# Optimization experiments

Measured on AMD Instinct MI355X. Metric: run time of the kernel, lower is better.

Reference implementation:

```python
import jax, jax.numpy as jnp
import numpy as np

K = 20000   # know_num
I = 50000   # item_num
D = 128     # emb_dim
N = K + I   # nodes in exer+know graphs (exercises first)
E1 = 320000 # edges in directed knowledge graph
E2 = 640000 # edges in each exer<->know graph


def setup_inputs() -> dict:
    key = jax.random.key(0)
    ks = jax.random.split(key, 20)
    s = 1.0 / np.sqrt(D)
    s2 = 1.0 / np.sqrt(2 * D)
    return {
        'kn_emb': jax.random.normal(ks[0], (K, D), jnp.float32),
        'exer_emb': jax.random.normal(ks[1], (I, D), jnp.float32),
        # GAT params: W is fc.weight.T ([in,out]); a is attn_fc.weight flattened ([2D])
        'W_dir': jax.random.normal(ks[2], (D, D), jnp.float32) * s,
        'a_dir': jax.random.normal(ks[3], (2 * D,), jnp.float32) * s2,
        'W_ke': jax.random.normal(ks[4], (D, D), jnp.float32) * s,
        'a_ke': jax.random.normal(ks[5], (2 * D,), jnp.float32) * s2,
        'W_ek': jax.random.normal(ks[6], (D, D), jnp.float32) * s,
        'a_ek': jax.random.normal(ks[7], (2 * D,), jnp.float32) * s2,
        # relation attention MLP: Linear(D,D)+bias, Tanh, Linear(D,1,no bias)
        'rel_W1': jax.random.normal(ks[8], (D, D), jnp.float32) * s,
        'rel_b1': jax.random.normal(ks[9], (D,), jnp.float32) * s,
        'rel_w2': jax.random.normal(ks[10], (D,), jnp.float32) * s,
        # edge lists (src, dst)
        'directed_src': jax.random.randint(ks[11], (E1,), 0, K),
        'directed_dst': jax.random.randint(ks[12], (E1,), 0, K),
        'ke_src': jax.random.randint(ks[13], (E2,), 0, N),
        'ke_dst': jax.random.randint(ks[14], (E2,), 0, N),
        'ek_src': jax.random.randint(ks[15], (E2,), 0, N),
        'ek_dst': jax.random.randint(ks[16], (E2,), 0, N),
    }


def _gat(h, W, a, src, dst, n):
    # GraphLayer: z = fc(h); e = leaky_relu(attn_fc([z_src; z_dst]));
    # alpha = softmax_e over dst; h_out = sum alpha * z_src
    z = h @ W                                   # [n_in, D]
    # split attn vector: cat([z_src,z_dst]) @ a == z_src@a[:D] + z_dst@a[D:]
    s_src = z @ a[:D]                           # [n_in]
    s_dst = z @ a[D:]                           # [n_in]
    e = jax.nn.leaky_relu(s_src[src] + s_dst[dst], 0.01)  # [E]
    m = jax.ops.segment_max(e, dst, num_segments=n)
    ex = jnp.exp(e - m[dst])
    den = jax.ops.segment_sum(ex, dst, num_segments=n)
    alpha = ex / den[dst]                       # segment softmax over in-edges
    return jax.ops.segment_sum(alpha[:, None] * z[src], dst, num_segments=n)


def reference(kn_emb, exer_emb, W_dir, a_dir, W_ke, a_ke, W_ek, a_ek,
              rel_W1, rel_b1, rel_w2,
              directed_src, directed_dst, ke_src, ke_dst, ek_src, ek_dst):
    A = _gat(kn_emb, W_dir, a_dir, directed_src, directed_dst, K)      # [K,D]
    ek = jnp.concatenate([exer_emb, kn_emb], axis=0)                   # [N,D]
    B = _gat(ek, W_ke, a_ke, ke_src, ke_dst, N)[I:]                    # [K,D]
    Cfull = _gat(ek, W_ek, a_ek, ek_src, ek_dst, N)                    # [N,D]
    s1 = jnp.tanh(A @ rel_W1 + rel_b1) @ rel_w2                        # [K]
    s2 = jnp.tanh(B @ rel_W1 + rel_b1) @ rel_w2                        # [K]
    score = jax.nn.softmax(jnp.stack([s1, s2], axis=1), axis=1)        # [K,2]
    kn_out = score[:, 0:1] * A + score[:, 1:2] * B                     # [K,D]
    exer_out = Cfull[:I]                                               # [I,D]
    return (kn_out, exer_out)
```

## Files before the change

kernel.cpp:

```cpp
#include <hip/hip_runtime.h>
#include <math.h>

#define KN   20000
#define IN_  50000
#define DD   128
#define NN   70000
#define E1N  320000
#define E2N  640000

#define GB0  313
#define GB1  1094
#define GB2  1094

typedef _Float16 f16x8 __attribute__((ext_vector_type(8)));
typedef float floatx4 __attribute__((ext_vector_type(4)));

__device__ __forceinline__ unsigned f2bf(float x) {
  unsigned u = __float_as_uint(x);
  return (u + 0x7FFFu + ((u >> 16) & 1u)) >> 16;
}
__device__ __forceinline__ unsigned packbf(float a, float b) {
  return f2bf(a) | (f2bf(b) << 16);
}
__device__ __forceinline__ float bf_lo(unsigned u) { return __uint_as_float(u << 16); }
__device__ __forceinline__ float bf_hi(unsigned u) { return __uint_as_float(u & 0xFFFF0000u); }

__global__ __launch_bounds__(256) void prep(
    const float* __restrict__ W0, const float* __restrict__ W1,
    const float* __restrict__ W2, const float* __restrict__ W3,
    short* __restrict__ wfr,
    const int* __restrict__ ddst, const int* __restrict__ kedst, const int* __restrict__ ekdst,
    int* __restrict__ cnt_dir, int* __restrict__ cnt_ke, int* __restrict__ cnt_ek,
    unsigned short* __restrict__ rank_dir, unsigned short* __restrict__ rank_ke,
    unsigned short* __restrict__ rank_ek)
{
  int b = blockIdx.x;
  if (b < 32) {
    int wsel = b >> 3;
    const float* W = (wsel == 0) ? W0 : (wsel == 1) ? W1 : (wsel == 2) ? W2 : W3;
    int fi = (b & 7) * 256 + threadIdx.x;
    int l = fi & 63, chunk = (fi >> 6) & 3, t = fi >> 8;
    int col = t * 16 + (l & 15);
    int kbase = chunk * 32 + (l >> 4) * 8;
    f16x8 hv;
#pragma unroll
    for (int j = 0; j < 8; ++j) hv[j] = (_Float16)W[(kbase + j) * 128 + col];
    ((f16x8*)(wfr + wsel * 16384))[fi] = hv;
    return;
  }
  int i = (b - 32) * 256 + threadIdx.x;
  if (i < E1N) {
    rank_dir[i] = (unsigned short)atomicAdd(&cnt_dir[ddst[i]], 1);
  } else if (i < E1N + E2N) {
    int e = i - E1N;
    int d = kedst[e];
    if (d >= IN_) rank_ke[e] = (unsigned short)atomicAdd(&cnt_ke[d - IN_], 1);
  } else {
    int e = i - E1N - E2N;
    int d = ekdst[e];
    if (d < IN_) rank_ek[e] = (unsigned short)atomicAdd(&cnt_ek[d], 1);
  }
}

__global__ __launch_bounds__(256, 4) void gemm3(
    const float* __restrict__ kn, const float* __restrict__ ex,
    const short* __restrict__ wfr,
    const float* __restrict__ a_dir, const float* __restrict__ a_ke, const float* __restrict__ a_ek,
    unsigned* __restrict__ zb_dir, unsigned* __restrict__ zb_ke, unsigned* __restrict__ zb_ek,
    float* __restrict__ sds, float* __restrict__ sdd,
    float* __restrict__ sks, float* __restrict__ skd,
    float* __restrict__ ses, float* __restrict__ sed)
{
  __shared__ short sW[16384];
  const int bid = blockIdx.x;
  const int tid = threadIdx.x;

  const float *h1, *h2, *avec;
  unsigned* zb;
  float *ssrc, *sdst;
  const short* wf;
  int split, rows, tile;
  if (bid < GB0) {
    tile = bid; rows = KN; split = KN; h1 = kn; h2 = kn;
    wf = wfr; avec = a_dir; zb = zb_dir; ssrc = sds; sdst = sdd;
  } else if (bid < GB0 + GB1) {
    tile = bid - GB0; rows = NN; split = IN_; h1 = ex; h2 = kn;
    wf = wfr + 16384; avec = a_ke; zb = zb_ke; ssrc = sks; sdst = skd;
  } else {
    tile = bid - GB0 - GB1; rows = NN; split = IN_; h1 = ex; h2 = kn;
    wf = wfr + 32768; avec = a_ek; zb = zb_ek; ssrc = ses; sdst = sed;
  }

  {
    const int4* gs = (const int4*)wf;
    int4* ls = (int4*)sW;
#pragma unroll
    for (int it = 0; it < 8; ++it) ls[it * 256 + tid] = gs[it * 256 + tid];
  }
  __syncthreads();

  const int lane = tid & 63;
  const int wv = tid >> 6;
  const int q = lane >> 4;
  const int m = lane & 15;
  const int r = tile * 64 + wv * 16 + m;
  const int rc = (r < rows) ? r : (rows - 1);
  const float* hp = (rc < split) ? (h1 + (size_t)rc * 128)
                                 : (h2 + (size_t)(rc - split) * 128);

  floatx4 acc[8];
#pragma unroll
  for (int t = 0; t < 8; ++t) { acc[t][0]=0.f; acc[t][1]=0.f; acc[t][2]=0.f; acc[t][3]=0.f; }

#pragma unroll
  for (int chunk = 0; chunk < 4; ++chunk) {
    float4 v0 = *(const float4*)(hp + chunk * 32 + q * 8);
    float4 v1 = *(const float4*)(hp + chunk * 32 + q * 8 + 4);
    float vs[8] = {v0.x, v0.y, v0.z, v0.w, v1.x, v1.y, v1.z, v1.w};
    f16x8 ahi, alo;
#pragma unroll
    for (int j = 0; j < 8; ++j) {
      _Float16 h = (_Float16)vs[j];
      ahi[j] = h;
      alo[j] = (_Float16)(vs[j] - (float)h);
    }
#pragma unroll
    for (int t = 0; t < 8; ++t) {
      f16x8 bh = ((const f16x8*)sW)[(t * 4 + chunk) * 64 + lane];
      acc[t] = __builtin_amdgcn_mfma_f32_16x16x32_f16(bh, ahi, acc[t], 0, 0, 0);
      acc[t] = __builtin_amdgcn_mfma_f32_16x16x32_f16(bh, alo, acc[t], 0, 0, 0);
    }
  }

  if (r < rows) {
    unsigned* zrow = zb + (size_t)r * 64;
#pragma unroll
    for (int t = 0; t < 8; ++t) {
      uint2 pk;
      pk.x = packbf(acc[t][0], acc[t][1]);
      pk.y = packbf(acc[t][2], acc[t][3]);
      *(uint2*)(zrow + t * 8 + q * 2) = pk;
    }
  }
  float d1 = 0.f, d2 = 0.f;
#pragma unroll
  for (int t = 0; t < 8; ++t) {
    float4 wa = *(const float4*)(avec + t * 16 + q * 4);
    float4 wb = *(const float4*)(avec + 128 + t * 16 + q * 4);
    d1 += acc[t][0] * wa.x + acc[t][1] * wa.y + acc[t][2] * wa.z + acc[t][3] * wa.w;
    d2 += acc[t][0] * wb.x + acc[t][1] * wb.y + acc[t][2] * wb.z + acc[t][3] * wb.w;
  }
  d1 += __shfl_xor(d1, 16, 64); d1 += __shfl_xor(d1, 32, 64);
  d2 += __shfl_xor(d2, 16, 64); d2 += __shfl_xor(d2, 32, 64);
  if (q == 0 && r < rows) { ssrc[r] = d1; sdst[r] = d2; }
}

__global__ __launch_bounds__(256) void alloc_off(
    const int* __restrict__ cnt_dir, int* __restrict__ st_dir,
    const int* __restrict__ cnt_ke,  int* __restrict__ st_ke,
    const int* __restrict__ cnt_ek,  int* __restrict__ st_ek,
    int* __restrict__ totals)
{
  int b = blockIdx.x;
  const int* cnt; int* st; int* tot; int n, i0;
  if (b < 79)       { cnt = cnt_dir; st = st_dir; tot = totals + 0; n = KN;  i0 = b * 256; }
  else if (b < 158) { cnt = cnt_ke;  st = st_ke;  tot = totals + 1; n = KN;  i0 = (b - 79) * 256; }
  else              { cnt = cnt_ek;  st = st_ek;  tot = totals + 2; n = IN_; i0 = (b - 158) * 256; }
  int i = i0 + threadIdx.x;
  int lane = threadIdx.x & 63;
  int v = (i < n) ? cnt[i] : 0;
  int x = v;
#pragma unroll
  for (int o = 1; o < 64; o <<= 1) {
    int t = __shfl_up(x, o, 64);
    if (lane >= o) x += t;
  }
  int base = 0;
  if (lane == 63) base = atomicAdd(tot, x);
  base = __shfl(base, 63, 64);
  if (i < n) st[i] = base + x - v;
}

__global__ __launch_bounds__(256) void fill_edges(
    const int* __restrict__ dsrc, const int* __restrict__ ddst,
    const int* __restrict__ kesrc, const int* __restrict__ kedst,
    const int* __restrict__ eksrc, const int* __restrict__ ekdst,
    const unsigned short* __restrict__ rank_dir, const unsigned short* __restrict__ rank_ke,
    const unsigned short* __restrict__ rank_ek,
    const float* __restrict__ sds, const float* __restrict__ sks, const float* __restrict__ ses,
    const int* __restrict__ st_dir, int2* __restrict__ ep_dir,
    const int* __restrict__ st_ke,  int2* __restrict__ ep_ke,
    const int* __restrict__ st_ek,  int2* __restrict__ ep_ek)
{
  int i = blockIdx.x * 256 + threadIdx.x;
  if (i < E1N) {
    int d = ddst[i];
    int s = dsrc[i];
    ep_dir[st_dir[d] + rank_dir[i]] = make_int2(s, __float_as_int(sds[s]));
  } else if (i < E1N + E2N) {
    int e = i - E1N;
    int d = kedst[e];
    if (d >= IN_) {
      int s = kesrc[e];
      ep_ke[st_ke[d - IN_] + rank_ke[e]] = make_int2(s, __float_as_int(sks[s]));
    }
  } else {
    int e = i - E1N - E2N;
    int d = ekdst[e];
    if (d < IN_) {
      int s = eksrc[e];
      ep_ek[st_ek[d] + rank_ek[e]] = make_int2(s, __float_as_int(ses[s]));
    }
  }
}

__global__ __launch_bounds__(256) void gat_gather(
    const int* __restrict__ st_dir, const int* __restrict__ cnt_dir, const int2* __restrict__ ep_dir,
    const float* __restrict__ sdd, const unsigned* __restrict__ zb_dir, float* __restrict__ A,
    const int* __restrict__ st_ke, const int* __restrict__ cnt_ke, const int2* __restrict__ ep_ke,
    const float* __restrict__ skd, const unsigned* __restrict__ zb_ke, float* __restrict__ Bm,
    const int* __restrict__ st_ek, const int* __restrict__ cnt_ek, const int2* __restrict__ ep_ek,
    const float* __restrict__ sed, const unsigned* __restrict__ zb_ek, float* __restrict__ Cout)
{
  int w = (blockIdx.x * 256 + threadIdx.x) >> 6;
  int lane = threadIdx.x & 63;
  int gid = lane >> 4, gl = lane & 15;
  const int *st, *cn; const int2* ep;
  const float* sD;
  const unsigned* zb;
  float* out;
  int seg, node;
  if (w < KN)                { seg = w;          node = seg;       st = st_dir; cn = cnt_dir; ep = ep_dir; sD = sdd; zb = zb_dir; out = A; }
  else if (w < 2 * KN)       { seg = w - KN;     node = seg + IN_; st = st_ke;  cn = cnt_ke;  ep = ep_ke;  sD = skd; zb = zb_ke;  out = Bm; }
  else if (w < 2 * KN + IN_) { seg = w - 2 * KN; node = seg;       st = st_ek;  cn = cnt_ek;  ep = ep_ek;  sD = sed; zb = zb_ek;  out = Cout; }
  else return;

  int b = st[seg], e = b + cn[seg];
  float av[8];
#pragma unroll
  for (int k = 0; k < 8; ++k) av[k] = 0.f;
  float den = 0.f;

  if (e > b) {
    float sd = sD[node];
    int i = b + gid;
    for (; i + 4 < e; i += 8) {
      int2 p1 = ep[i], p2 = ep[i + 4];
      float x1 = __int_as_float(p1.y) + sd; x1 = (x1 > 0.f) ? x1 : 0.01f * x1;
      float x2 = __int_as_float(p2.y) + sd; x2 = (x2 > 0.f) ? x2 : 0.01f * x2;
      float w1 = __expf(x1), w2 = __expf(x2);
      uint4 za = *(const uint4*)(zb + (size_t)p1.x * 64 + gl * 4);
      uint4 zc = *(const uint4*)(zb + (size_t)p2.x * 64 + gl * 4);
      den += w1 + w2;
      av[0] += w1 * bf_lo(za.x); av[1] += w1 * bf_hi(za.x);
      av[2] += w1 * bf_lo(za.y); av[3] += w1 * bf_hi(za.y);
      av[4] += w1 * bf_lo(za.z); av[5] += w1 * bf_hi(za.z);
      av[6] += w1 * bf_lo(za.w); av[7] += w1 * bf_hi(za.w);
      av[0] += w2 * bf_lo(zc.x); av[1] += w2 * bf_hi(zc.x);
      av[2] += w2 * bf_lo(zc.y); av[3] += w2 * bf_hi(zc.y);
      av[4] += w2 * bf_lo(zc.z); av[5] += w2 * bf_hi(zc.z);
      av[6] += w2 * bf_lo(zc.w); av[7] += w2 * bf_hi(zc.w);
    }
    if (i < e) {
      int2 p1 = ep[i];
      float x1 = __int_as_float(p1.y) + sd; x1 = (x1 > 0.f) ? x1 : 0.01f * x1;
      float w1 = __expf(x1);
      uint4 za = *(const uint4*)(zb + (size_t)p1.x * 64 + gl * 4);
      den += w1;
      av[0] += w1 * bf_lo(za.x); av[1] += w1 * bf_hi(za.x);
      av[2] += w1 * bf_lo(za.y); av[3] += w1 * bf_hi(za.y);
      av[4] += w1 * bf_lo(za.z); av[5] += w1 * bf_hi(za.z);
      av[6] += w1 * bf_lo(za.w); av[7] += w1 * bf_hi(za.w);
    }
    den += __shfl_xor(den, 16, 64);
    den += __shfl_xor(den, 32, 64);
#pragma unroll
    for (int k = 0; k < 8; ++k) {
      av[k] += __shfl_xor(av[k], 16, 64);
      av[k] += __shfl_xor(av[k], 32, 64);
    }
    float inv = 1.f / den;
#pragma unroll
    for (int k = 0; k < 8; ++k) av[k] *= inv;
  }

  if (gid == 0) {
    float* op = out + (size_t)seg * 128 + gl * 8;
    *(float4*)op       = make_float4(av[0], av[1], av[2], av[3]);
    *(float4*)(op + 4) = make_float4(av[4], av[5], av[6], av[7]);
  }
}

__global__ __launch_bounds__(256, 2) void relgemm_combine(
    const float* __restrict__ Am, const float* __restrict__ Bm,
    const short* __restrict__ wfr_rel,
    const float* __restrict__ rb1, const float* __restrict__ rw2,
    float* __restrict__ out)
{
  __shared__ short sW[16384];
  const int tid = threadIdx.x;
  {
    const int4* gs = (const int4*)wfr_rel;
    int4* ls = (int4*)sW;
#pragma unroll
    for (int it = 0; it < 8; ++it) ls[it * 256 + tid] = gs[it * 256 + tid];
  }
  __syncthreads();

  const int lane = tid & 63;
  const int wv = tid >> 6;
  const int q = lane >> 4;
  const int m = lane & 15;
  const int r = blockIdx.x * 64 + wv * 16 + m;
  const int rc = (r < KN) ? r : (KN - 1);
  const float* hA = Am + (size_t)rc * 128;
  const float* hB = Bm + (size_t)rc * 128;

  floatx4 accA[8], accB[8];
#pragma unroll
  for (int t = 0; t < 8; ++t) {
    accA[t][0]=0.f; accA[t][1]=0.f; accA[t][2]=0.f; accA[t][3]=0.f;
    accB[t][0]=0.f; accB[t][1]=0.f; accB[t][2]=0.f; accB[t][3]=0.f;
  }

#pragma unroll
  for (int chunk = 0; chunk < 4; ++chunk) {
    float4 a0 = *(const float4*)(hA + chunk * 32 + q * 8);
    float4 a1 = *(const float4*)(hA + chunk * 32 + q * 8 + 4);
    float4 b0 = *(const float4*)(hB + chunk * 32 + q * 8);
    float4 b1 = *(const float4*)(hB + chunk * 32 + q * 8 + 4);
    float as[8] = {a0.x, a0.y, a0.z, a0.w, a1.x, a1.y, a1.z, a1.w};
    float bs[8] = {b0.x, b0.y, b0.z, b0.w, b1.x, b1.y, b1.z, b1.w};
    f16x8 ahiA, aloA, ahiB, aloB;
#pragma unroll
    for (int j = 0; j < 8; ++j) {
      _Float16 ha = (_Float16)as[j];
      ahiA[j] = ha; aloA[j] = (_Float16)(as[j] - (float)ha);
      _Float16 hb = (_Float16)bs[j];
      ahiB[j] = hb; aloB[j] = (_Float16)(bs[j] - (float)hb);
    }
#pragma unroll
    for (int t = 0; t < 8; ++t) {
      f16x8 bh = ((const f16x8*)sW)[(t * 4 + chunk) * 64 + lane];
      accA[t] = __builtin_amdgcn_mfma_f32_16x16x32_f16(bh, ahiA, accA[t], 0, 0, 0);
      accA[t] = __builtin_amdgcn_mfma_f32_16x16x32_f16(bh, aloA, accA[t], 0, 0, 0);
      accB[t] = __builtin_amdgcn_mfma_f32_16x16x32_f16(bh, ahiB, accB[t], 0, 0, 0);
      accB[t] = __builtin_amdgcn_mfma_f32_16x16x32_f16(bh, aloB, accB[t], 0, 0, 0);
    }
  }

  float p1 = 0.f, p2 = 0.f;
#pragma unroll
  for (int t = 0; t < 8; ++t) {
    float4 bb = *(const float4*)(rb1 + t * 16 + q * 4);
    float4 ww = *(const float4*)(rw2 + t * 16 + q * 4);
    p1 += tanhf(accA[t][0] + bb.x) * ww.x + tanhf(accA[t][1] + bb.y) * ww.y +
          tanhf(accA[t][2] + bb.z) * ww.z + tanhf(accA[t][3] + bb.w) * ww.w;
    p2 += tanhf(accB[t][0] + bb.x) * ww.x + tanhf(accB[t][1] + bb.y) * ww.y +
          tanhf(accB[t][2] + bb.z) * ww.z + tanhf(accB[t][3] + bb.w) * ww.w;
  }
  p1 += __shfl_xor(p1, 16, 64); p1 += __shfl_xor(p1, 32, 64);
  p2 += __shfl_xor(p2, 16, 64); p2 += __shfl_xor(p2, 32, 64);

  float mx = fmaxf(p1, p2);
  float e1 = __expf(p1 - mx), e2 = __expf(p2 - mx);
  float al = e1 / (e1 + e2), be = e2 / (e1 + e2);

  if (r < KN) {
#pragma unroll
    for (int t = 0; t < 8; ++t) {
      int col = t * 16 + q * 4;
      float4 avv = *(const float4*)(Am + (size_t)r * 128 + col);
      float4 bvv = *(const float4*)(Bm + (size_t)r * 128 + col);
      *(float4*)(out + (size_t)r * 128 + col) =
          make_float4(al * avv.x + be * bvv.x, al * avv.y + be * bvv.y,
                      al * avv.z + be * bvv.z, al * avv.w + be * bvv.w);
    }
  }
}

extern "C" void kernel_launch(void* const* d_in, const int* in_sizes, int n_in,
                              void* d_out, int out_size, void* d_ws, size_t ws_size,
                              hipStream_t stream) {
  const float* kn    = (const float*)d_in[0];
  const float* ex    = (const float*)d_in[1];
  const float* W_dir = (const float*)d_in[2];
  const float* a_dir = (const float*)d_in[3];
  const float* W_ke  = (const float*)d_in[4];
  const float* a_ke  = (const float*)d_in[5];
  const float* W_ek  = (const float*)d_in[6];
  const float* a_ek  = (const float*)d_in[7];
  const float* rW1   = (const float*)d_in[8];
  const float* rb1   = (const float*)d_in[9];
  const float* rw2   = (const float*)d_in[10];
  const int* dsrc    = (const int*)d_in[11];
  const int* ddst    = (const int*)d_in[12];
  const int* kesrc   = (const int*)d_in[13];
  const int* kedst   = (const int*)d_in[14];
  const int* eksrc   = (const int*)d_in[15];
  const int* ekdst   = (const int*)d_in[16];
  float* out = (float*)d_out;

  char* p = (char*)d_ws;
  auto alloc = [&](size_t bytes) {
    char* r = p;
    p += (bytes + 255) & ~(size_t)255;
    return r;
  };
  unsigned* zb_dir = (unsigned*)alloc((size_t)KN * 64 * 4);
  unsigned* zb_ke  = (unsigned*)alloc((size_t)NN * 64 * 4);
  unsigned* zb_ek  = (unsigned*)alloc((size_t)NN * 64 * 4);
  float* Am    = (float*)alloc((size_t)KN * 128 * 4);
  float* Bmat  = (float*)alloc((size_t)KN * 128 * 4);
  short* wfr   = (short*)alloc((size_t)4 * 16384 * 2);
  float* sds = (float*)alloc(KN * 4);
  float* sdd = (float*)alloc(KN * 4);
  float* sks = (float*)alloc(NN * 4);
  float* skd = (float*)alloc(NN * 4);
  float* ses = (float*)alloc(NN * 4);
  float* sed = (float*)alloc(NN * 4);
  int* cntblk  = (int*)alloc((size_t)(2 * KN + IN_ + 64) * 4);
  int* cnt_dir = cntblk;
  int* cnt_ke  = cntblk + KN;
  int* cnt_ek  = cntblk + 2 * KN;
  int* totals  = cntblk + 2 * KN + IN_;
  int* st_dir = (int*)alloc(KN * 4);
  int* st_ke  = (int*)alloc(KN * 4);
  int* st_ek  = (int*)alloc(IN_ * 4);
  unsigned short* rank_dir = (unsigned short*)alloc((size_t)E1N * 2);
  unsigned short* rank_ke  = (unsigned short*)alloc((size_t)E2N * 2);
  unsigned short* rank_ek  = (unsigned short*)alloc((size_t)E2N * 2);
  int2* ep_dir = (int2*)alloc((size_t)E1N * 8);
  int2* ep_ke  = (int2*)alloc((size_t)E2N * 8);
  int2* ep_ek  = (int2*)alloc((size_t)E2N * 8);

  hipMemsetAsync(cntblk, 0, (size_t)(2 * KN + IN_ + 64) * 4, stream);

  prep<<<32 + (E1N + 2 * E2N) / 256, 256, 0, stream>>>(
      W_dir, W_ke, W_ek, rW1, wfr,
      ddst, kedst, ekdst, cnt_dir, cnt_ke, cnt_ek,
      rank_dir, rank_ke, rank_ek);

  gemm3<<<GB0 + GB1 + GB2, 256, 0, stream>>>(
      kn, ex, wfr, a_dir, a_ke, a_ek,
      zb_dir, zb_ke, zb_ek,
      sds, sdd, sks, skd, ses, sed);

  alloc_off<<<354, 256, 0, stream>>>(cnt_dir, st_dir, cnt_ke, st_ke, cnt_ek, st_ek, totals);

  fill_edges<<<(E1N + 2 * E2N) / 256, 256, 0, stream>>>(
      dsrc, ddst, kesrc, kedst, eksrc, ekdst,
      rank_dir, rank_ke, rank_ek,
      sds, sks, ses,
      st_dir, ep_dir, st_ke, ep_ke, st_ek, ep_ek);

  gat_gather<<<(2 * KN + IN_) / 4, 256, 0, stream>>>(
      st_dir, cnt_dir, ep_dir, sdd, zb_dir, Am,
      st_ke,  cnt_ke,  ep_ke,  skd, zb_ke,  Bmat,
      st_ek,  cnt_ek,  ep_ek,  sed, zb_ek,  out + (size_t)KN * 128);

  relgemm_combine<<<313, 256, 0, stream>>>(Am, Bmat, wfr + 3 * 16384, rb1, rw2, out);
}
```

Measured before the change: 283.6 us.

## Precompute edge softmax weights in fill and gather with 16-lane groups per segment

fill_edges now evaluates leaky_relu and exp per edge using both source and destination scores, and stores the final weight in the edge record. This removes the destination-score lookup and exp from the gather. gat_gather switches from one wavefront per destination segment (four interleaved edge streams plus shuffle reductions) to one 16-lane group per segment. Each group walks its edges serially with 16-byte paired edge loads, packed float2 accumulation and no cross-lane reduction. relgemm_combine keeps the A/B row values it already loaded in registers for the final blend instead of reloading them, at the cost of more register pressure.

```diff
diff --git a/kernel.cpp b/kernel.cpp
--- a/kernel.cpp
+++ b/kernel.cpp
@@ -14,6 +14,7 @@
 
 typedef _Float16 f16x8 __attribute__((ext_vector_type(8)));
 typedef float floatx4 __attribute__((ext_vector_type(4)));
+typedef float floatx2 __attribute__((ext_vector_type(2)));
 
 __device__ __forceinline__ unsigned f2bf(float x) {
   unsigned u = __float_as_uint(x);
@@ -24,6 +25,9 @@
 }
 __device__ __forceinline__ float bf_lo(unsigned u) { return __uint_as_float(u << 16); }
 __device__ __forceinline__ float bf_hi(unsigned u) { return __uint_as_float(u & 0xFFFF0000u); }
+__device__ __forceinline__ floatx2 bfp(unsigned u) {
+  floatx2 r; r.x = bf_lo(u); r.y = bf_hi(u); return r;
+}
 
 __global__ __launch_bounds__(256) void prep(
     const float* __restrict__ W0, const float* __restrict__ W1,
@@ -187,7 +191,9 @@
     const int* __restrict__ eksrc, const int* __restrict__ ekdst,
     const unsigned short* __restrict__ rank_dir, const unsigned short* __restrict__ rank_ke,
     const unsigned short* __restrict__ rank_ek,
-    const float* __restrict__ sds, const float* __restrict__ sks, const float* __restrict__ ses,
+    const float* __restrict__ sds, const float* __restrict__ sdd,
+    const float* __restrict__ sks, const float* __restrict__ skd,
+    const float* __restrict__ ses, const float* __restrict__ sed,
     const int* __restrict__ st_dir, int2* __restrict__ ep_dir,
     const int* __restrict__ st_ke,  int2* __restrict__ ep_ke,
     const int* __restrict__ st_ek,  int2* __restrict__ ep_ek)
@@ -196,99 +202,84 @@
   if (i < E1N) {
     int d = ddst[i];
     int s = dsrc[i];
-    ep_dir[st_dir[d] + rank_dir[i]] = make_int2(s, __float_as_int(sds[s]));
+    float x = sds[s] + sdd[d];
+    x = (x > 0.f) ? x : 0.01f * x;
+    ep_dir[st_dir[d] + rank_dir[i]] = make_int2(s, __float_as_int(__expf(x)));
   } else if (i < E1N + E2N) {
     int e = i - E1N;
     int d = kedst[e];
     if (d >= IN_) {
       int s = kesrc[e];
-      ep_ke[st_ke[d - IN_] + rank_ke[e]] = make_int2(s, __float_as_int(sks[s]));
+      float x = sks[s] + skd[d];
+      x = (x > 0.f) ? x : 0.01f * x;
+      ep_ke[st_ke[d - IN_] + rank_ke[e]] = make_int2(s, __float_as_int(__expf(x)));
     }
   } else {
     int e = i - E1N - E2N;
     int d = ekdst[e];
     if (d < IN_) {
       int s = eksrc[e];
-      ep_ek[st_ek[d] + rank_ek[e]] = make_int2(s, __float_as_int(ses[s]));
+      float x = ses[s] + sed[d];
+      x = (x > 0.f) ? x : 0.01f * x;
+      ep_ek[st_ek[d] + rank_ek[e]] = make_int2(s, __float_as_int(__expf(x)));
     }
   }
 }
 
 __global__ __launch_bounds__(256) void gat_gather(
     const int* __restrict__ st_dir, const int* __restrict__ cnt_dir, const int2* __restrict__ ep_dir,
-    const float* __restrict__ sdd, const unsigned* __restrict__ zb_dir, float* __restrict__ A,
+    const unsigned* __restrict__ zb_dir, float* __restrict__ A,
     const int* __restrict__ st_ke, const int* __restrict__ cnt_ke, const int2* __restrict__ ep_ke,
-    const float* __restrict__ skd, const unsigned* __restrict__ zb_ke, float* __restrict__ Bm,
+    const unsigned* __restrict__ zb_ke, float* __restrict__ Bm,
     const int* __restrict__ st_ek, const int* __restrict__ cnt_ek, const int2* __restrict__ ep_ek,
-    const float* __restrict__ sed, const unsigned* __restrict__ zb_ek, float* __restrict__ Cout)
-{
-  int w = (blockIdx.x * 256 + threadIdx.x) >> 6;
-  int lane = threadIdx.x & 63;
-  int gid = lane >> 4, gl = lane & 15;
+    const unsigned* __restrict__ zb_ek, float* __restrict__ Cout)
+{
+  int g = (blockIdx.x * 256 + threadIdx.x) >> 4;
+  int gl = threadIdx.x & 15;
   const int *st, *cn; const int2* ep;
-  const float* sD;
   const unsigned* zb;
   float* out;
-  int seg, node;
-  if (w < KN)                { seg = w;          node = seg;       st = st_dir; cn = cnt_dir; ep = ep_dir; sD = sdd; zb = zb_dir; out = A; }
-  else if (w < 2 * KN)       { seg = w - KN;     node = seg + IN_; st = st_ke;  cn = cnt_ke;  ep = ep_ke;  sD = skd; zb = zb_ke;  out = Bm; }
-  else if (w < 2 * KN + IN_) { seg = w - 2 * KN; node = seg;       st = st_ek;  cn = cnt_ek;  ep = ep_ek;  sD = sed; zb = zb_ek;  out = Cout; }
+  int seg;
+  if (g < KN)                { seg = g;          st = st_dir; cn = cnt_dir; ep = ep_dir; zb = zb_dir; out = A; }
+  else if (g < 2 * KN)       { seg = g - KN;     st = st_ke;  cn = cnt_ke;  ep = ep_ke;  zb = zb_ke;  out = Bm; }
+  else if (g < 2 * KN + IN_) { seg = g - 2 * KN; st = st_ek;  cn = cnt_ek;  ep = ep_ek;  zb = zb_ek;  out = Cout; }
   else return;
 
-  int b = st[seg], e = b + cn[seg];
-  float av[8];
-#pragma unroll
-  for (int k = 0; k < 8; ++k) av[k] = 0.f;
+  int b = st[seg], n = cn[seg], e = b + n;
+  floatx2 av0, av1, av2, av3;
+  av0 = 0.f; av1 = 0.f; av2 = 0.f; av3 = 0.f;
   float den = 0.f;
 
-  if (e > b) {
-    float sd = sD[node];
-    int i = b + gid;
-    for (; i + 4 < e; i += 8) {
-      int2 p1 = ep[i], p2 = ep[i + 4];
-      float x1 = __int_as_float(p1.y) + sd; x1 = (x1 > 0.f) ? x1 : 0.01f * x1;
-      float x2 = __int_as_float(p2.y) + sd; x2 = (x2 > 0.f) ? x2 : 0.01f * x2;
-      float w1 = __expf(x1), w2 = __expf(x2);
-      uint4 za = *(const uint4*)(zb + (size_t)p1.x * 64 + gl * 4);
-      uint4 zc = *(const uint4*)(zb + (size_t)p2.x * 64 + gl * 4);
-      den += w1 + w2;
-      av[0] += w1 * bf_lo(za.x); av[1] += w1 * bf_hi(za.x);
-      av[2] += w1 * bf_lo(za.y); av[3] += w1 * bf_hi(za.y);
-      av[4] += w1 * bf_lo(za.z); av[5] += w1 * bf_hi(za.z);
-      av[6] += w1 * bf_lo(za.w); av[7] += w1 * bf_hi(za.w);
-      av[0] += w2 * bf_lo(zc.x); av[1] += w2 * bf_hi(zc.x);
-      av[2] += w2 * bf_lo(zc.y); av[3] += w2 * bf_hi(zc.y);
-      av[4] += w2 * bf_lo(zc.z); av[5] += w2 * bf_hi(zc.z);
-      av[6] += w2 * bf_lo(zc.w); av[7] += w2 * bf_hi(zc.w);
-    }
-    if (i < e) {
-      int2 p1 = ep[i];
-      float x1 = __int_as_float(p1.y) + sd; x1 = (x1 > 0.f) ? x1 : 0.01f * x1;
-      float w1 = __expf(x1);
-      uint4 za = *(const uint4*)(zb + (size_t)p1.x * 64 + gl * 4);
-      den += w1;
-      av[0] += w1 * bf_lo(za.x); av[1] += w1 * bf_hi(za.x);
-      av[2] += w1 * bf_lo(za.y); av[3] += w1 * bf_hi(za.y);
-      av[4] += w1 * bf_lo(za.z); av[5] += w1 * bf_hi(za.z);
-      av[6] += w1 * bf_lo(za.w); av[7] += w1 * bf_hi(za.w);
-    }
-    den += __shfl_xor(den, 16, 64);
-    den += __shfl_xor(den, 32, 64);
-#pragma unroll
-    for (int k = 0; k < 8; ++k) {
-      av[k] += __shfl_xor(av[k], 16, 64);
-      av[k] += __shfl_xor(av[k], 32, 64);
-    }
-    float inv = 1.f / den;
-#pragma unroll
-    for (int k = 0; k < 8; ++k) av[k] *= inv;
-  }
-
-  if (gid == 0) {
-    float* op = out + (size_t)seg * 128 + gl * 8;
-    *(float4*)op       = make_float4(av[0], av[1], av[2], av[3]);
-    *(float4*)(op + 4) = make_float4(av[4], av[5], av[6], av[7]);
-  }
+  int i = b;
+  for (; i + 3 < e; i += 4) {
+    int4 pa = *(const int4*)(ep + i);
+    int4 pb = *(const int4*)(ep + i + 2);
+    uint4 z0 = *(const uint4*)(zb + (size_t)pa.x * 64 + gl * 4);
+    uint4 z1 = *(const uint4*)(zb + (size_t)pa.z * 64 + gl * 4);
+    uint4 z2 = *(const uint4*)(zb + (size_t)pb.x * 64 + gl * 4);
+    uint4 z3 = *(const uint4*)(zb + (size_t)pb.z * 64 + gl * 4);
+    float w0 = __int_as_float(pa.y), w1 = __int_as_float(pa.w);
+    float w2 = __int_as_float(pb.y), w3 = __int_as_float(pb.w);
+    den += (w0 + w1) + (w2 + w3);
+    av0 += bfp(z0.x) * w0; av1 += bfp(z0.y) * w0; av2 += bfp(z0.z) * w0; av3 += bfp(z0.w) * w0;
+    av0 += bfp(z1.x) * w1; av1 += bfp(z1.y) * w1; av2 += bfp(z1.z) * w1; av3 += bfp(z1.w) * w1;
+    av0 += bfp(z2.x) * w2; av1 += bfp(z2.y) * w2; av2 += bfp(z2.z) * w2; av3 += bfp(z2.w) * w2;
+    av0 += bfp(z3.x) * w3; av1 += bfp(z3.y) * w3; av2 += bfp(z3.z) * w3; av3 += bfp(z3.w) * w3;
+  }
+  for (; i < e; ++i) {
+    int2 pe = ep[i];
+    uint4 z = *(const uint4*)(zb + (size_t)pe.x * 64 + gl * 4);
+    float w = __int_as_float(pe.y);
+    den += w;
+    av0 += bfp(z.x) * w; av1 += bfp(z.y) * w; av2 += bfp(z.z) * w; av3 += bfp(z.w) * w;
+  }
+
+  float inv = (n > 0) ? 1.f / den : 0.f;
+  av0 *= inv; av1 *= inv; av2 *= inv; av3 *= inv;
+
+  float* op = out + (size_t)seg * 128 + gl * 8;
+  *(float4*)op       = make_float4(av0.x, av0.y, av1.x, av1.y);
+  *(float4*)(op + 4) = make_float4(av2.x, av2.y, av3.x, av3.y);
 }
 
 __global__ __launch_bounds__(256, 2) void relgemm_combine(
@@ -323,21 +314,26 @@
     accB[t][0]=0.f; accB[t][1]=0.f; accB[t][2]=0.f; accB[t][3]=0.f;
   }
 
+  float asv[4][8], bsv[4][8];
+
 #pragma unroll
   for (int chunk = 0; chunk < 4; ++chunk) {
     float4 a0 = *(const float4*)(hA + chunk * 32 + q * 8);
     float4 a1 = *(const float4*)(hA + chunk * 32 + q * 8 + 4);
     float4 b0 = *(const float4*)(hB + chunk * 32 + q * 8);
     float4 b1 = *(const float4*)(hB + chunk * 32 + q * 8 + 4);
-    float as[8] = {a0.x, a0.y, a0.z, a0.w, a1.x, a1.y, a1.z, a1.w};
-    float bs[8] = {b0.x, b0.y, b0.z, b0.w, b1.x, b1.y, b1.z, b1.w};
+    asv[chunk][0]=a0.x; asv[chunk][1]=a0.y; asv[chunk][2]=a0.z; asv[chunk][3]=a0.w;
+    asv[chunk][4]=a1.x; asv[chunk][5]=a1.y; asv[chunk][6]=a1.z; asv[chunk][7]=a1.w;
+    bsv[chunk][0]=b0.x; bsv[chunk][1]=b0.y; bsv[chunk][2]=b0.z; bsv[chunk][3]=b0.w;
+    bsv[chunk][4]=b1.x; bsv[chunk][5]=b1.y; bsv[chunk][6]=b1.z; bsv[chunk][7]=b1.w;
     f16x8 ahiA, aloA, ahiB, aloB;
 #pragma unroll
     for (int j = 0; j < 8; ++j) {
-      _Float16 ha = (_Float16)as[j];
-      ahiA[j] = ha; aloA[j] = (_Float16)(as[j] - (float)ha);
-      _Float16 hb = (_Float16)bs[j];
-      ahiB[j] = hb; aloB[j] = (_Float16)(bs[j] - (float)hb);
+      float a = asv[chunk][j], bvl = bsv[chunk][j];
+      _Float16 ha = (_Float16)a;
+      ahiA[j] = ha; aloA[j] = (_Float16)(a - (float)ha);
+      _Float16 hb = (_Float16)bvl;
+      ahiB[j] = hb; aloB[j] = (_Float16)(bvl - (float)hb);
     }
 #pragma unroll
     for (int t = 0; t < 8; ++t) {
@@ -368,13 +364,13 @@
 
   if (r < KN) {
 #pragma unroll
-    for (int t = 0; t < 8; ++t) {
-      int col = t * 16 + q * 4;
-      float4 avv = *(const float4*)(Am + (size_t)r * 128 + col);
-      float4 bvv = *(const float4*)(Bm + (size_t)r * 128 + col);
-      *(float4*)(out + (size_t)r * 128 + col) =
-          make_float4(al * avv.x + be * bvv.x, al * avv.y + be * bvv.y,
-                      al * avv.z + be * bvv.z, al * avv.w + be * bvv.w);
+    for (int chunk = 0; chunk < 4; ++chunk) {
+      float o[8];
+#pragma unroll
+      for (int j = 0; j < 8; ++j) o[j] = al * asv[chunk][j] + be * bsv[chunk][j];
+      float* op = out + (size_t)r * 128 + chunk * 32 + q * 8;
+      *(float4*)op       = make_float4(o[0], o[1], o[2], o[3]);
+      *(float4*)(op + 4) = make_float4(o[4], o[5], o[6], o[7]);
     }
   }
 }
@@ -451,13 +447,13 @@
   fill_edges<<<(E1N + 2 * E2N) / 256, 256, 0, stream>>>(
       dsrc, ddst, kesrc, kedst, eksrc, ekdst,
       rank_dir, rank_ke, rank_ek,
-      sds, sks, ses,
+      sds, sdd, sks, skd, ses, sed,
       st_dir, ep_dir, st_ke, ep_ke, st_ek, ep_ek);
 
-  gat_gather<<<(2 * KN + IN_) / 4, 256, 0, stream>>>(
-      st_dir, cnt_dir, ep_dir, sdd, zb_dir, Am,
-      st_ke,  cnt_ke,  ep_ke,  skd, zb_ke,  Bmat,
-      st_ek,  cnt_ek,  ep_ek,  sed, zb_ek,  out + (size_t)KN * 128);
+  gat_gather<<<(2 * KN + IN_) / 16, 256, 0, stream>>>(
+      st_dir, cnt_dir, ep_dir, zb_dir, Am,
+      st_ke,  cnt_ke,  ep_ke,  zb_ke,  Bmat,
+      st_ek,  cnt_ek,  ep_ek,  zb_ek,  out + (size_t)KN * 128);
 
   relgemm_combine<<<313, 256, 0, stream>>>(Am, Bmat, wfr + 3 * 16384, rb1, rw2, out);
 }
```

Measured after the change: 289.0 us. About the same (+1.9%).
